# Kernel tuning notes

Hardware: AMD Instinct MI355X
Metric: run time of the kernel (lower is better)

Reference implementation:

```python
import jax, jax.numpy as jnp
import numpy as np

H, KVH, HD = 16, 8, 64
EPS = 1e-6
SCALING = HD ** -0.5


def _rms_norm(x, w):
    # RMSNorm over last dim (head_dim)
    var = jnp.mean(x * x, axis=-1, keepdims=True)
    return x * jax.lax.rsqrt(var + EPS) * w


def _rotate_half(x):
    x1, x2 = jnp.split(x, 2, axis=-1)
    return jnp.concatenate([-x2, x1], axis=-1)


def setup_inputs() -> dict:
    key = jax.random.key(0)
    ks = jax.random.split(key, 12)
    B, Q, CTX, HID = 1, 2048, 2048, 1024
    NB, T = 32, 64  # Q == NB * T
    TOTAL = CTX + Q
    inp = {}
    inp["hidden_states"] = jax.random.normal(ks[0], (B, Q, HID), jnp.float32)
    inp["target_hidden"] = jax.random.normal(ks[1], (B, CTX, HID), jnp.float32)
    pos = jnp.arange(TOTAL, dtype=jnp.float32)[:, None]
    inv = 1.0 / (10000.0 ** (jnp.arange(0, HD, 2, dtype=jnp.float32) / HD))
    ang = pos * inv[None, :]
    emb = jnp.concatenate([ang, ang], axis=-1)
    inp["cos"] = jnp.cos(emb)[None]  # [B, TOTAL, HD]
    inp["sin"] = jnp.sin(emb)[None]
    inp["attention_mask"] = jnp.zeros((B, 1, Q, TOTAL), jnp.float32)
    s = 0.02
    inp["Wq"] = jax.random.normal(ks[2], (HID, H * HD), jnp.float32) * s
    inp["Wk"] = jax.random.normal(ks[3], (HID, KVH * HD), jnp.float32) * s
    inp["Wv"] = jax.random.normal(ks[4], (HID, KVH * HD), jnp.float32) * s
    inp["Wo"] = jax.random.normal(ks[5], (H * HD, HID), jnp.float32) * s
    inp["q_norm_w"] = jnp.ones((HD,), jnp.float32)
    inp["k_norm_w"] = jnp.ones((HD,), jnp.float32)
    inp["tree_bias"] = jax.random.normal(ks[6], (64, H), jnp.float32) * s
    inp["relation_map"] = jax.random.randint(ks[7], (B, NB, T, T), 0, 64, jnp.int32)
    return inp


def reference(hidden_states, target_hidden, cos, sin, attention_mask,
              Wq, Wk, Wv, Wo, q_norm_w, k_norm_w, tree_bias, relation_map):
    B, Q, HID = hidden_states.shape
    CTX = target_hidden.shape[1]
    TOTAL = CTX + Q
    NB, T = relation_map.shape[1], relation_map.shape[2]
    groups = H // KVH

    q = (hidden_states @ Wq).reshape(B, Q, H, HD)
    k_ctx = target_hidden @ Wk
    k_noise = hidden_states @ Wk
    v_ctx = target_hidden @ Wv
    v_noise = hidden_states @ Wv
    k = jnp.concatenate([k_ctx, k_noise], axis=1).reshape(B, TOTAL, KVH, HD)
    v = jnp.concatenate([v_ctx, v_noise], axis=1).reshape(B, TOTAL, KVH, HD)

    q = _rms_norm(q, q_norm_w).transpose(0, 2, 1, 3)  # [B,H,Q,HD]
    k = _rms_norm(k, k_norm_w).transpose(0, 2, 1, 3)  # [B,KVH,TOTAL,HD]
    v = v.transpose(0, 2, 1, 3)

    cos_b = cos[:, None]  # [B,1,TOTAL,HD]
    sin_b = sin[:, None]
    q = q * cos_b[..., -Q:, :] + _rotate_half(q) * sin_b[..., -Q:, :]
    k = k * cos_b + _rotate_half(k) * sin_b

    # GQA: repeat kv heads
    k = jnp.repeat(k, groups, axis=1)  # [B,H,TOTAL,HD]
    v = jnp.repeat(v, groups, axis=1)

    scores = jnp.einsum('bhqd,bhkd->bhqk', q, k) * SCALING  # [B,H,Q,TOTAL]
    scores = scores + attention_mask

    # tree positional bias: block-diagonal (same tree) on the noise-noise block
    bias = tree_bias[relation_map]                 # [B,NB,T,T,H]
    bias = jnp.transpose(bias, (0, 4, 1, 2, 3))    # [B,H,NB,T,T]
    s_noise = scores[..., CTX:].reshape(B, H, NB, T, NB, T)
    idx = jnp.arange(NB)
    s_noise = s_noise.at[:, :, idx, :, idx, :].add(jnp.transpose(bias, (2, 0, 1, 3, 4)))
    scores = jnp.concatenate([scores[..., :CTX], s_noise.reshape(B, H, Q, Q)], axis=-1)

    attn = jax.nn.softmax(scores, axis=-1)
    out = jnp.einsum('bhqk,bhkd->bhqd', attn, v)   # [B,H,Q,HD]
    out = out.transpose(0, 2, 1, 3).reshape(B, Q, H * HD)
    return out @ Wo
```

## Files before the change

kernel.cpp:

```cpp
#include <hip/hip_runtime.h>
#include <hip/hip_bf16.h>

typedef __bf16 bf16x8 __attribute__((ext_vector_type(8)));
typedef float  f32x4  __attribute__((ext_vector_type(4)));

__device__ inline unsigned short f2bf(float f) {
    unsigned int u = __float_as_uint(f);
    u += 0x7fffu + ((u >> 16) & 1u);
    return (unsigned short)(u >> 16);
}
__device__ inline float bf2f(unsigned int s) {
    return __uint_as_float(s << 16);
}
__device__ inline unsigned int pk2bf(float a, float b) {
    __hip_bfloat162 h = __float22bfloat162_rn(make_float2(a, b));
    union { __hip_bfloat162 h; unsigned int u; } cv;
    cv.h = h;
    return cv.u;
}
__device__ inline f32x4 mfma16(bf16x8 a, bf16x8 b, f32x4 c) {
    return __builtin_amdgcn_mfma_f32_16x16x32_bf16(a, b, c, 0, 0, 0);
}
__device__ inline void gload_lds16(const void* g, void* l) {
    __builtin_amdgcn_global_load_lds(
        (const __attribute__((address_space(1))) void*)g,
        (__attribute__((address_space(3))) void*)l, 16, 0, 0);
}

__global__ __launch_bounds__(256) void cast2_bf(const float* __restrict__ a,
                                                const float* __restrict__ b,
                                                unsigned short* __restrict__ out, int n4each) {
    int i = blockIdx.x * 256 + threadIdx.x;
    float4 v = (i < n4each) ? ((const float4*)a)[i] : ((const float4*)b)[i - n4each];
    ((uint2*)out)[i] = make_uint2(pk2bf(v.x, v.y), pk2bf(v.z, v.w));
}

__global__ __launch_bounds__(256) void trans4v(const float* __restrict__ Wk,
                                               const float* __restrict__ Wv,
                                               const float* __restrict__ Wq,
                                               const float* __restrict__ Wo,
                                               unsigned short* __restrict__ Wkvt,
                                               unsigned short* __restrict__ Wqt,
                                               unsigned short* __restrict__ Wot) {
    __shared__ float t[64][65];
    int z = blockIdx.z;
    const float* in;
    unsigned short* out;
    int in_rs;
    if (z == 0)      { if (blockIdx.x >= 8) return; in = Wk; out = Wkvt; in_rs = 512; }
    else if (z == 1) { if (blockIdx.x >= 8) return; in = Wv; out = Wkvt + (size_t)512 * 1024; in_rs = 512; }
    else if (z == 2) { in = Wq; out = Wqt; in_rs = 1024; }
    else             { in = Wo; out = Wot; in_rs = 1024; }
    int r0 = blockIdx.y * 64, c0b = blockIdx.x * 64;
    int tid = threadIdx.x, rr = tid >> 4, c4 = (tid & 15) * 4;
#pragma unroll
    for (int i = 0; i < 4; i++) {
        int r = rr + 16 * i;
        float4 v = *(const float4*)&in[(size_t)(r0 + r) * in_rs + c0b + c4];
        t[c4][r] = v.x; t[c4 + 1][r] = v.y; t[c4 + 2][r] = v.z; t[c4 + 3][r] = v.w;
    }
    __syncthreads();
#pragma unroll
    for (int i = 0; i < 4; i++) {
        int cc = rr + 16 * i;
        *(uint2*)&out[(size_t)(c0b + cc) * 1024 + r0 + c4] =
            make_uint2(pk2bf(t[cc][c4], t[cc][c4 + 1]), pk2bf(t[cc][c4 + 2], t[cc][c4 + 3]));
    }
}

__global__ __launch_bounds__(256) void vtrans2(const unsigned short* __restrict__ in,
                                               unsigned short* __restrict__ out) {
    __shared__ float t[64][65];
    const unsigned short* ip = in + (size_t)blockIdx.y * 64 + (size_t)blockIdx.x * 64 * 1024;
    unsigned short* op = out + (size_t)blockIdx.y * 64 * 4096 + blockIdx.x * 64;
    int tid = threadIdx.x, rr = tid >> 4, c0 = (tid & 15) * 4;
#pragma unroll
    for (int i = 0; i < 4; i++) {
        int r = rr + 16 * i;
        uint2 v = *(const uint2*)&ip[(size_t)r * 1024 + c0];
        t[c0][r] = bf2f(v.x & 0xffff); t[c0 + 1][r] = bf2f(v.x >> 16);
        t[c0 + 2][r] = bf2f(v.y & 0xffff); t[c0 + 3][r] = bf2f(v.y >> 16);
    }
    __syncthreads();
#pragma unroll
    for (int i = 0; i < 4; i++) {
        int d = rr + 16 * i;
        *(uint2*)&op[(size_t)d * 4096 + c0] =
            make_uint2(pk2bf(t[d][c0], t[d][c0 + 1]), pk2bf(t[d][c0 + 2], t[d][c0 + 3]));
    }
}

template <bool BF16OUT>
__device__ inline void gemm64_body(const unsigned short* __restrict__ A,
                                   const unsigned short* __restrict__ Bt,
                                   void* __restrict__ C, int m0, int n0,
                                   unsigned short (*Al)[128 * 32],
                                   unsigned short (*Bl)[64 * 32]) {
    int tid = threadIdx.x, wave = tid >> 6, lane = tid & 63, quad = lane >> 4, l16 = lane & 15;
    f32x4 acc[2][4] = {};

    int dr = lane >> 2;
    int sch = ((lane & 3) ^ (dr & 3)) * 8;
    const unsigned short* Ag0 = A + (size_t)(m0 + 32 * wave + dr) * 1024 + sch;
    const unsigned short* Ag1 = A + (size_t)(m0 + 32 * wave + 16 + dr) * 1024 + sch;
    const unsigned short* Bg  = Bt + (size_t)(n0 + 16 * wave + dr) * 1024 + sch;

    auto dma = [&](int k0, int b) {
        gload_lds16(Ag0 + k0, (char*)Al[b] + wave * 2048);
        gload_lds16(Ag1 + k0, (char*)Al[b] + wave * 2048 + 1024);
        gload_lds16(Bg + k0, (char*)Bl[b] + wave * 1024);
    };
    dma(0, 0);
    int swz = (quad ^ (l16 & 3)) * 8;

    for (int k0 = 0; k0 < 1024; k0 += 32) {
        __syncthreads();
        int b = (k0 >> 5) & 1;
        if (k0 + 32 < 1024) dma(k0 + 32, b ^ 1);
        bf16x8 af[2], bq[4];
#pragma unroll
        for (int i = 0; i < 2; i++)
            af[i] = *(const bf16x8*)&Al[b][(wave * 32 + i * 16 + l16) * 32 + swz];
#pragma unroll
        for (int j = 0; j < 4; j++)
            bq[j] = *(const bf16x8*)&Bl[b][(j * 16 + l16) * 32 + swz];
#pragma unroll
        for (int i = 0; i < 2; i++)
#pragma unroll
            for (int j = 0; j < 4; j++)
                acc[i][j] = mfma16(af[i], bq[j], acc[i][j]);
    }
#pragma unroll
    for (int i = 0; i < 2; i++)
#pragma unroll
        for (int j = 0; j < 4; j++) {
            int m = m0 + wave * 32 + i * 16 + quad * 4;
            int n = n0 + j * 16 + l16;
#pragma unroll
            for (int r = 0; r < 4; r++) {
                if constexpr (BF16OUT)
                    ((unsigned short*)C)[(size_t)(m + r) * 1024 + n] = f2bf(acc[i][j][r]);
                else
                    ((float*)C)[(size_t)(m + r) * 1024 + n] = acc[i][j][r];
            }
        }
}

__global__ __launch_bounds__(256) void gemm_qkv(const unsigned short* __restrict__ X,
                                                const unsigned short* __restrict__ Wkvt,
                                                const unsigned short* __restrict__ Wqt,
                                                unsigned short* __restrict__ KVraw,
                                                unsigned short* __restrict__ Qraw) {
    __shared__ unsigned short Al[2][128 * 32];
    __shared__ unsigned short Bl[2][64 * 32];
    int bx = blockIdx.x, n0 = blockIdx.y * 64;
    if (bx < 32) gemm64_body<true>(X, Wkvt, KVraw, bx * 128, n0, Al, Bl);
    else         gemm64_body<true>(X + (size_t)2048 * 1024, Wqt, Qraw, (bx - 32) * 128, n0, Al, Bl);
}

__global__ __launch_bounds__(256) void gemm_wo(const unsigned short* __restrict__ A,
                                               const unsigned short* __restrict__ Bt,
                                               float* __restrict__ C) {
    __shared__ unsigned short Al[2][128 * 32];
    __shared__ unsigned short Bl[2][64 * 32];
    gemm64_body<false>(A, Bt, C, blockIdx.x * 128, blockIdx.y * 64, Al, Bl);
}

__global__ __launch_bounds__(256) void norm_rope3(const unsigned short* __restrict__ Qraw,
                                                  const unsigned short* __restrict__ KVraw,
                                                  const float* __restrict__ qw,
                                                  const float* __restrict__ kw,
                                                  const float* __restrict__ cosb,
                                                  const float* __restrict__ sinb,
                                                  unsigned short* __restrict__ Qb,
                                                  unsigned short* __restrict__ Kb) {
    int gw = (blockIdx.x * 256 + threadIdx.x) >> 6;
    int lane = threadIdx.x & 63;
    int hl = lane >> 4, d0 = (lane & 15) * 4;
    const unsigned short* src;
    unsigned short* dst;
    const float* w;
    int pos;
    float scale;
    if (gw < 8192) {
        int r = gw >> 2, seg = gw & 3, h = seg * 4 + hl;
        src = Qraw + (size_t)r * 1024 + h * 64 + d0;
        dst = Qb + ((size_t)h * 2048 + r) * 64 + d0;
        w = qw; pos = 2048 + r; scale = 0.18033688011112042f;
    } else {
        int g2 = gw - 8192;
        int r = g2 >> 1, seg = g2 & 1, h = seg * 4 + hl;
        src = KVraw + (size_t)r * 1024 + h * 64 + d0;
        dst = Kb + ((size_t)h * 4096 + r) * 64 + d0;
        w = kw; pos = r; scale = 1.0f;
    }
    uint2 raw = *(const uint2*)src;
    float x0 = bf2f(raw.x & 0xffff), x1 = bf2f(raw.x >> 16);
    float x2 = bf2f(raw.y & 0xffff), x3 = bf2f(raw.y >> 16);
    float ss = x0 * x0 + x1 * x1 + x2 * x2 + x3 * x3;
    ss += __shfl_xor(ss, 1); ss += __shfl_xor(ss, 2);
    ss += __shfl_xor(ss, 4); ss += __shfl_xor(ss, 8);
    float rn = rsqrtf(ss * (1.0f / 64.0f) + 1e-6f);
    float4 wv = *(const float4*)(w + d0);
    float xn0 = x0 * rn * wv.x, xn1 = x1 * rn * wv.y;
    float xn2 = x2 * rn * wv.z, xn3 = x3 * rn * wv.w;
    float o0 = __shfl_xor(xn0, 8), o1 = __shfl_xor(xn1, 8);
    float o2 = __shfl_xor(xn2, 8), o3 = __shfl_xor(xn3, 8);
    float sgn = (d0 < 32) ? -1.0f : 1.0f;
    float4 cv = *(const float4*)(cosb + (size_t)pos * 64 + d0);
    float4 sv = *(const float4*)(sinb + (size_t)pos * 64 + d0);
    float y0 = fmaf(xn0, cv.x, sgn * o0 * sv.x) * scale;
    float y1 = fmaf(xn1, cv.y, sgn * o1 * sv.y) * scale;
    float y2 = fmaf(xn2, cv.z, sgn * o2 * sv.z) * scale;
    float y3 = fmaf(xn3, cv.w, sgn * o3 * sv.w) * scale;
    *(uint2*)dst = make_uint2(pk2bf(y0, y1), pk2bf(y2, y3));
}

__global__ __launch_bounds__(256) void attn4(const unsigned short* __restrict__ Qb,
                                             const unsigned short* __restrict__ Kb,
                                             const unsigned short* __restrict__ Vt,
                                             const int* __restrict__ relmap,
                                             const float* __restrict__ tree_bias,
                                             unsigned short* __restrict__ Opart,
                                             float* __restrict__ Lpart) {
    __shared__ alignas(16) union {
        struct { unsigned short K[2][4096]; unsigned short V[2][4096]; unsigned short P[4][32 * 72]; } s;
        unsigned short O[128 * 72];
    } u;

    int qt = blockIdx.x, h = blockIdx.y, ks = blockIdx.z, kvh = h >> 1;
    int tid = threadIdx.x, wave = tid >> 6, lane = tid & 63, quad = lane >> 4, l16 = lane & 15;

    bf16x8 qf[2][2];
#pragma unroll
    for (int qg = 0; qg < 2; qg++) {
        int q = qt * 128 + wave * 32 + qg * 16 + l16;
        const unsigned short* qp = Qb + ((size_t)h * 2048 + q) * 64 + quad * 8;
        qf[qg][0] = *(const bf16x8*)qp;
        qf[qg][1] = *(const bf16x8*)(qp + 32);
    }
    f32x4 o[4][2] = {};
    f32x4 lacc[2] = {};

    union { unsigned short us[8]; bf16x8 v; } one_u;
#pragma unroll
    for (int i = 0; i < 8; i++) one_u.us[i] = 0x3F80;
    const bf16x8 ones = one_u.v;

    int drow = lane >> 3;
    int sch = ((lane & 7) ^ drow) * 8;
    const unsigned short* KgB = Kb + ((size_t)kvh * 4096 + ks * 1024) * 64;
    const unsigned short* VgB = Vt + (size_t)kvh * 64 * 4096 + ks * 1024;
    int r0 = wave * 16, r1 = wave * 16 + 8;
    const unsigned short* Kg0 = KgB + (size_t)(r0 + drow) * 64 + sch;
    const unsigned short* Kg1 = KgB + (size_t)(r1 + drow) * 64 + sch;
    const unsigned short* Vg0 = VgB + (size_t)(r0 + drow) * 4096 + sch;
    const unsigned short* Vg1 = VgB + (size_t)(r1 + drow) * 4096 + sch;

    auto dma = [&](int kt, int b) {
        gload_lds16(Kg0 + kt * 4096, &u.s.K[b][r0 * 64]);
        gload_lds16(Kg1 + kt * 4096, &u.s.K[b][r1 * 64]);
        gload_lds16(Vg0 + kt * 64, &u.s.V[b][r0 * 64]);
        gload_lds16(Vg1 + kt * 64, &u.s.V[b][r1 * 64]);
    };
    dma(0, 0);

    unsigned short* pw = &u.s.P[wave][0];
    int sw = l16 & 7;
    int nb = 2 * qt + (wave >> 1);
    int bias_kt = 32 + nb - ks * 16;
    const float LOG2E = 1.4426950408889634f;

    for (int kt = 0; kt < 16; kt++) {
        __syncthreads();
        int b = kt & 1;
        if (kt + 1 < 16) dma(kt + 1, b ^ 1);

#pragma unroll
        for (int half = 0; half < 2; half++) {
            float pvv[2][2][4];
#pragma unroll
            for (int gl = 0; gl < 2; gl++) {
                int g = half * 2 + gl;
                int krow = (g * 16 + l16) * 64;
                bf16x8 kf0 = *(const bf16x8*)&u.s.K[b][krow + ((quad ^ sw) * 8)];
                bf16x8 kf1 = *(const bf16x8*)&u.s.K[b][krow + (((4 + quad) ^ sw) * 8)];
#pragma unroll
                for (int qg = 0; qg < 2; qg++) {
                    f32x4 s = {};
                    s = mfma16(kf0, qf[qg][0], s);
                    s = mfma16(kf1, qf[qg][1], s);
#pragma unroll
                    for (int r = 0; r < 4; r++) pvv[gl][qg][r] = s[r];
                }
            }
            if (kt == bias_kt) {
#pragma unroll
                for (int gl = 0; gl < 2; gl++)
#pragma unroll
                    for (int qg = 0; qg < 2; qg++)
#pragma unroll
                        for (int r = 0; r < 4; r++) {
                            int t1 = (wave & 1) * 32 + qg * 16 + l16;
                            int t2 = (half * 2 + gl) * 16 + quad * 4 + r;
                            int rel = relmap[nb * 4096 + t1 * 64 + t2];
                            pvv[gl][qg][r] += tree_bias[rel * 16 + h] * LOG2E;
                        }
            }
#pragma unroll
            for (int gl = 0; gl < 2; gl++)
#pragma unroll
                for (int qg = 0; qg < 2; qg++) {
                    float p0 = __builtin_amdgcn_exp2f(pvv[gl][qg][0]);
                    float p1 = __builtin_amdgcn_exp2f(pvv[gl][qg][1]);
                    float p2 = __builtin_amdgcn_exp2f(pvv[gl][qg][2]);
                    float p3 = __builtin_amdgcn_exp2f(pvv[gl][qg][3]);
                    *(uint2*)&pw[(qg * 16 + l16) * 72 + (half * 2 + gl) * 16 + quad * 4] =
                        make_uint2(pk2bf(p0, p1), pk2bf(p2, p3));
                }
#pragma unroll
            for (int qg = 0; qg < 2; qg++) {
                bf16x8 pf = *(const bf16x8*)&pw[(qg * 16 + l16) * 72 + half * 32 + quad * 8];
                lacc[qg] = mfma16(ones, pf, lacc[qg]);
#pragma unroll
                for (int dg = 0; dg < 4; dg++) {
                    int vrow = (dg * 16 + l16) * 64;
                    bf16x8 vf = *(const bf16x8*)&u.s.V[b][vrow + (((half * 4 + quad) ^ sw) * 8)];
                    o[dg][qg] = mfma16(vf, pf, o[dg][qg]);
                }
            }
        }
    }
    __syncthreads();

    float lv0 = lacc[0][0], lv1 = lacc[1][0];
#pragma unroll
    for (int qg = 0; qg < 2; qg++) {
        int qlocal = wave * 32 + qg * 16 + l16;
#pragma unroll
        for (int dg = 0; dg < 4; dg++) {
            f32x4 ov = o[dg][qg];
            *(uint2*)&u.O[qlocal * 72 + dg * 16 + quad * 4] =
                make_uint2(pk2bf(ov[0], ov[1]), pk2bf(ov[2], ov[3]));
        }
        if (quad == 0)
            Lpart[((size_t)ks * 16 + h) * 2048 + qt * 128 + qlocal] = qg ? lv1 : lv0;
    }
    __syncthreads();
    int row = tid >> 3, c = (tid & 7) * 8;
#pragma unroll
    for (int i = 0; i < 4; i++) {
        int rr = row + 32 * i;
        uint4 val = *(uint4*)&u.O[rr * 72 + c];
        size_t q = qt * 128 + rr;
        *(uint4*)&Opart[((size_t)ks * 2048 + q) * 1024 + h * 64 + c] = val;
    }
}

__global__ __launch_bounds__(256) void combine4(const unsigned short* __restrict__ Op,
                                                const float* __restrict__ Lp,
                                                unsigned short* __restrict__ AO) {
    int t = blockIdx.x * 256 + threadIdx.x;
    int q = t >> 7, h = (t >> 3) & 15, c8 = (t & 7) * 8;
    size_t base = ((size_t)q * 16 + h) * 64 + c8;
    float s[8] = {};
    float l = 0.0f;
#pragma unroll
    for (int ks = 0; ks < 4; ks++) {
        uint4 v = *(const uint4*)&Op[(size_t)ks * 2097152 + base];
        s[0] += bf2f(v.x & 0xffff); s[1] += bf2f(v.x >> 16);
        s[2] += bf2f(v.y & 0xffff); s[3] += bf2f(v.y >> 16);
        s[4] += bf2f(v.z & 0xffff); s[5] += bf2f(v.z >> 16);
        s[6] += bf2f(v.w & 0xffff); s[7] += bf2f(v.w >> 16);
        l += Lp[((size_t)ks * 16 + h) * 2048 + q];
    }
    float inv = 1.0f / l;
    uint4 r;
    r.x = pk2bf(s[0] * inv, s[1] * inv);
    r.y = pk2bf(s[2] * inv, s[3] * inv);
    r.z = pk2bf(s[4] * inv, s[5] * inv);
    r.w = pk2bf(s[6] * inv, s[7] * inv);
    *(uint4*)&AO[base] = r;
}

extern "C" void kernel_launch(void* const* d_in, const int* in_sizes, int n_in,
                              void* d_out, int out_size, void* d_ws, size_t ws_size,
                              hipStream_t stream) {
    const float* hs   = (const float*)d_in[0];
    const float* th   = (const float*)d_in[1];
    const float* cosb = (const float*)d_in[2];
    const float* sinb = (const float*)d_in[3];
    const float* Wq  = (const float*)d_in[5];
    const float* Wk  = (const float*)d_in[6];
    const float* Wv  = (const float*)d_in[7];
    const float* Wo  = (const float*)d_in[8];
    const float* qnw = (const float*)d_in[9];
    const float* knw = (const float*)d_in[10];
    const float* tb  = (const float*)d_in[11];
    const int*   rm  = (const int*)d_in[12];
    float* out = (float*)d_out;

    char* ws = (char*)d_ws;
    size_t off = 0;
    auto alloc = [&](size_t b) { char* p = ws + off; off += (b + 255) & ~(size_t)255; return p; };
    unsigned short* X     = (unsigned short*)alloc((size_t)4096 * 1024 * 2);
    unsigned short* Qrawb = (unsigned short*)alloc((size_t)2048 * 1024 * 2);
    unsigned short* KVraw = (unsigned short*)alloc((size_t)4096 * 1024 * 2);
    unsigned short* Wqt   = (unsigned short*)alloc((size_t)1024 * 1024 * 2);
    unsigned short* Wkvt  = (unsigned short*)alloc((size_t)1024 * 1024 * 2);
    unsigned short* Wot   = (unsigned short*)alloc((size_t)1024 * 1024 * 2);
    unsigned short* Qb    = (unsigned short*)alloc((size_t)16 * 2048 * 64 * 2);
    unsigned short* Kb    = (unsigned short*)alloc((size_t)8 * 4096 * 64 * 2);
    unsigned short* Vtr   = (unsigned short*)alloc((size_t)8 * 64 * 4096 * 2);
    unsigned short* AOb   = (unsigned short*)alloc((size_t)2048 * 1024 * 2);
    float*          Lpart = (float*)alloc((size_t)4 * 16 * 2048 * 4);
    unsigned short* Opart = X;

    cast2_bf<<<4096, 256, 0, stream>>>(th, hs, X, 2048 * 1024 / 4);
    trans4v<<<dim3(16, 16, 4), 256, 0, stream>>>(Wk, Wv, Wq, Wo, Wkvt, Wqt, Wot);
    gemm_qkv<<<dim3(48, 16), 256, 0, stream>>>(X, Wkvt, Wqt, KVraw, Qrawb);
    norm_rope3<<<4096, 256, 0, stream>>>(Qrawb, KVraw, qnw, knw, cosb, sinb, Qb, Kb);
    vtrans2<<<dim3(64, 8), 256, 0, stream>>>(KVraw + 512, Vtr);
    attn4<<<dim3(16, 16, 4), 256, 0, stream>>>(Qb, Kb, Vtr, rm, tb, Opart, Lpart);
    combine4<<<1024, 256, 0, stream>>>(Opart, Lpart, AOb);
    gemm_wo<<<dim3(16, 16), 256, 0, stream>>>(AOb, Wot, out);
}
```

Before: 228.3 us.

## Merge prep kernels and load V fragments directly from global in attention

Result: slower. 262.7 us (+15.1%).

```diff
diff --git a/kernel.cpp b/kernel.cpp
--- a/kernel.cpp
+++ b/kernel.cpp
@@ -27,32 +27,30 @@
         (__attribute__((address_space(3))) void*)l, 16, 0, 0);
 }
 
-__global__ __launch_bounds__(256) void cast2_bf(const float* __restrict__ a,
-                                                const float* __restrict__ b,
-                                                unsigned short* __restrict__ out, int n4each) {
-    int i = blockIdx.x * 256 + threadIdx.x;
-    float4 v = (i < n4each) ? ((const float4*)a)[i] : ((const float4*)b)[i - n4each];
-    ((uint2*)out)[i] = make_uint2(pk2bf(v.x, v.y), pk2bf(v.z, v.w));
-}
-
-__global__ __launch_bounds__(256) void trans4v(const float* __restrict__ Wk,
-                                               const float* __restrict__ Wv,
-                                               const float* __restrict__ Wq,
-                                               const float* __restrict__ Wo,
-                                               unsigned short* __restrict__ Wkvt,
-                                               unsigned short* __restrict__ Wqt,
-                                               unsigned short* __restrict__ Wot) {
+__global__ __launch_bounds__(256) void prep1(const float* __restrict__ th, const float* __restrict__ hs,
+                                             const float* __restrict__ Wk, const float* __restrict__ Wv,
+                                             const float* __restrict__ Wq, const float* __restrict__ Wo,
+                                             unsigned short* __restrict__ X,
+                                             unsigned short* __restrict__ Wkvt,
+                                             unsigned short* __restrict__ Wqt,
+                                             unsigned short* __restrict__ Wot) {
     __shared__ float t[64][65];
-    int z = blockIdx.z;
-    const float* in;
-    unsigned short* out;
-    int in_rs;
-    if (z == 0)      { if (blockIdx.x >= 8) return; in = Wk; out = Wkvt; in_rs = 512; }
-    else if (z == 1) { if (blockIdx.x >= 8) return; in = Wv; out = Wkvt + (size_t)512 * 1024; in_rs = 512; }
-    else if (z == 2) { in = Wq; out = Wqt; in_rs = 1024; }
-    else             { in = Wo; out = Wot; in_rs = 1024; }
-    int r0 = blockIdx.y * 64, c0b = blockIdx.x * 64;
-    int tid = threadIdx.x, rr = tid >> 4, c4 = (tid & 15) * 4;
+    int bx = blockIdx.x, tid = threadIdx.x;
+    if (bx < 4096) {
+        int i = bx * 256 + tid;
+        const int n4 = 2048 * 1024 / 4;
+        float4 v = (i < n4) ? ((const float4*)th)[i] : ((const float4*)hs)[i - n4];
+        ((uint2*)X)[i] = make_uint2(pk2bf(v.x, v.y), pk2bf(v.z, v.w));
+        return;
+    }
+    int t4 = bx - 4096;
+    const float* in; unsigned short* out; int in_rs, xt, yt;
+    if (t4 < 256)      { in = Wq; out = Wqt; in_rs = 1024; xt = t4 & 15; yt = t4 >> 4; }
+    else if (t4 < 512) { t4 -= 256; in = Wo; out = Wot; in_rs = 1024; xt = t4 & 15; yt = t4 >> 4; }
+    else if (t4 < 640) { t4 -= 512; in = Wk; out = Wkvt; in_rs = 512; xt = t4 & 7; yt = t4 >> 3; }
+    else               { t4 -= 640; in = Wv; out = Wkvt + (size_t)512 * 1024; in_rs = 512; xt = t4 & 7; yt = t4 >> 3; }
+    int r0 = yt * 64, c0b = xt * 64;
+    int rr = tid >> 4, c4 = (tid & 15) * 4;
 #pragma unroll
     for (int i = 0; i < 4; i++) {
         int r = rr + 16 * i;
@@ -68,34 +66,12 @@
     }
 }
 
-__global__ __launch_bounds__(256) void vtrans2(const unsigned short* __restrict__ in,
-                                               unsigned short* __restrict__ out) {
-    __shared__ float t[64][65];
-    const unsigned short* ip = in + (size_t)blockIdx.y * 64 + (size_t)blockIdx.x * 64 * 1024;
-    unsigned short* op = out + (size_t)blockIdx.y * 64 * 4096 + blockIdx.x * 64;
-    int tid = threadIdx.x, rr = tid >> 4, c0 = (tid & 15) * 4;
-#pragma unroll
-    for (int i = 0; i < 4; i++) {
-        int r = rr + 16 * i;
-        uint2 v = *(const uint2*)&ip[(size_t)r * 1024 + c0];
-        t[c0][r] = bf2f(v.x & 0xffff); t[c0 + 1][r] = bf2f(v.x >> 16);
-        t[c0 + 2][r] = bf2f(v.y & 0xffff); t[c0 + 3][r] = bf2f(v.y >> 16);
-    }
-    __syncthreads();
-#pragma unroll
-    for (int i = 0; i < 4; i++) {
-        int d = rr + 16 * i;
-        *(uint2*)&op[(size_t)d * 4096 + c0] =
-            make_uint2(pk2bf(t[d][c0], t[d][c0 + 1]), pk2bf(t[d][c0 + 2], t[d][c0 + 3]));
-    }
-}
-
 template <bool BF16OUT>
-__device__ inline void gemm64_body(const unsigned short* __restrict__ A,
-                                   const unsigned short* __restrict__ Bt,
-                                   void* __restrict__ C, int m0, int n0,
-                                   unsigned short (*Al)[128 * 32],
-                                   unsigned short (*Bl)[64 * 32]) {
+__device__ __forceinline__ void gemm64_body(const unsigned short* __restrict__ A,
+                                            const unsigned short* __restrict__ Bt,
+                                            void* __restrict__ C, int m0, int n0,
+                                            unsigned short (*Al)[128 * 32],
+                                            unsigned short (*Bl)[64 * 32]) {
     int tid = threadIdx.x, wave = tid >> 6, lane = tid & 63, quad = lane >> 4, l16 = lane & 15;
     f32x4 acc[2][4] = {};
 
@@ -166,65 +142,90 @@
     gemm64_body<false>(A, Bt, C, blockIdx.x * 128, blockIdx.y * 64, Al, Bl);
 }
 
-__global__ __launch_bounds__(256) void norm_rope3(const unsigned short* __restrict__ Qraw,
-                                                  const unsigned short* __restrict__ KVraw,
-                                                  const float* __restrict__ qw,
-                                                  const float* __restrict__ kw,
-                                                  const float* __restrict__ cosb,
-                                                  const float* __restrict__ sinb,
-                                                  unsigned short* __restrict__ Qb,
-                                                  unsigned short* __restrict__ Kb) {
-    int gw = (blockIdx.x * 256 + threadIdx.x) >> 6;
-    int lane = threadIdx.x & 63;
-    int hl = lane >> 4, d0 = (lane & 15) * 4;
-    const unsigned short* src;
-    unsigned short* dst;
-    const float* w;
-    int pos;
-    float scale;
-    if (gw < 8192) {
-        int r = gw >> 2, seg = gw & 3, h = seg * 4 + hl;
-        src = Qraw + (size_t)r * 1024 + h * 64 + d0;
-        dst = Qb + ((size_t)h * 2048 + r) * 64 + d0;
-        w = qw; pos = 2048 + r; scale = 0.18033688011112042f;
-    } else {
-        int g2 = gw - 8192;
-        int r = g2 >> 1, seg = g2 & 1, h = seg * 4 + hl;
-        src = KVraw + (size_t)r * 1024 + h * 64 + d0;
-        dst = Kb + ((size_t)h * 4096 + r) * 64 + d0;
-        w = kw; pos = r; scale = 1.0f;
-    }
-    uint2 raw = *(const uint2*)src;
-    float x0 = bf2f(raw.x & 0xffff), x1 = bf2f(raw.x >> 16);
-    float x2 = bf2f(raw.y & 0xffff), x3 = bf2f(raw.y >> 16);
-    float ss = x0 * x0 + x1 * x1 + x2 * x2 + x3 * x3;
-    ss += __shfl_xor(ss, 1); ss += __shfl_xor(ss, 2);
-    ss += __shfl_xor(ss, 4); ss += __shfl_xor(ss, 8);
-    float rn = rsqrtf(ss * (1.0f / 64.0f) + 1e-6f);
-    float4 wv = *(const float4*)(w + d0);
-    float xn0 = x0 * rn * wv.x, xn1 = x1 * rn * wv.y;
-    float xn2 = x2 * rn * wv.z, xn3 = x3 * rn * wv.w;
-    float o0 = __shfl_xor(xn0, 8), o1 = __shfl_xor(xn1, 8);
-    float o2 = __shfl_xor(xn2, 8), o3 = __shfl_xor(xn3, 8);
-    float sgn = (d0 < 32) ? -1.0f : 1.0f;
-    float4 cv = *(const float4*)(cosb + (size_t)pos * 64 + d0);
-    float4 sv = *(const float4*)(sinb + (size_t)pos * 64 + d0);
-    float y0 = fmaf(xn0, cv.x, sgn * o0 * sv.x) * scale;
-    float y1 = fmaf(xn1, cv.y, sgn * o1 * sv.y) * scale;
-    float y2 = fmaf(xn2, cv.z, sgn * o2 * sv.z) * scale;
-    float y3 = fmaf(xn3, cv.w, sgn * o3 * sv.w) * scale;
-    *(uint2*)dst = make_uint2(pk2bf(y0, y1), pk2bf(y2, y3));
-}
-
-__global__ __launch_bounds__(256) void attn4(const unsigned short* __restrict__ Qb,
-                                             const unsigned short* __restrict__ Kb,
-                                             const unsigned short* __restrict__ Vt,
-                                             const int* __restrict__ relmap,
-                                             const float* __restrict__ tree_bias,
-                                             unsigned short* __restrict__ Opart,
-                                             float* __restrict__ Lpart) {
+__global__ __launch_bounds__(256) void prep2(const unsigned short* __restrict__ Qraw,
+                                             const unsigned short* __restrict__ KVraw,
+                                             const float* __restrict__ qw, const float* __restrict__ kw,
+                                             const float* __restrict__ cosb, const float* __restrict__ sinb,
+                                             unsigned short* __restrict__ Qb,
+                                             unsigned short* __restrict__ Kb,
+                                             unsigned short* __restrict__ Vtr) {
+    __shared__ float t[64][65];
+    int bx = blockIdx.x, tid = threadIdx.x;
+    if (bx < 4096) {
+        int gw = (bx * 256 + tid) >> 6;
+        int lane = tid & 63;
+        int hl = lane >> 4, d0 = (lane & 15) * 4;
+        const unsigned short* src;
+        unsigned short* dst;
+        const float* w;
+        int pos;
+        float scale;
+        if (gw < 8192) {
+            int r = gw >> 2, seg = gw & 3, h = seg * 4 + hl;
+            src = Qraw + (size_t)r * 1024 + h * 64 + d0;
+            dst = Qb + ((size_t)h * 2048 + r) * 64 + d0;
+            w = qw; pos = 2048 + r; scale = 0.18033688011112042f;
+        } else {
+            int g2 = gw - 8192;
+            int r = g2 >> 1, seg = g2 & 1, h = seg * 4 + hl;
+            src = KVraw + (size_t)r * 1024 + h * 64 + d0;
+            dst = Kb + ((size_t)h * 4096 + r) * 64 + d0;
+            w = kw; pos = r; scale = 1.0f;
+        }
+        uint2 raw = *(const uint2*)src;
+        float x0 = bf2f(raw.x & 0xffff), x1 = bf2f(raw.x >> 16);
+        float x2 = bf2f(raw.y & 0xffff), x3 = bf2f(raw.y >> 16);
+        float ss = x0 * x0 + x1 * x1 + x2 * x2 + x3 * x3;
+        ss += __shfl_xor(ss, 1); ss += __shfl_xor(ss, 2);
+        ss += __shfl_xor(ss, 4); ss += __shfl_xor(ss, 8);
+        float rn = rsqrtf(ss * (1.0f / 64.0f) + 1e-6f);
+        float4 wv = *(const float4*)(w + d0);
+        float xn0 = x0 * rn * wv.x, xn1 = x1 * rn * wv.y;
+        float xn2 = x2 * rn * wv.z, xn3 = x3 * rn * wv.w;
+        float o0 = __shfl_xor(xn0, 8), o1 = __shfl_xor(xn1, 8);
+        float o2 = __shfl_xor(xn2, 8), o3 = __shfl_xor(xn3, 8);
+        float sgn = (d0 < 32) ? -1.0f : 1.0f;
+        float4 cv = *(const float4*)(cosb + (size_t)pos * 64 + d0);
+        float4 sv = *(const float4*)(sinb + (size_t)pos * 64 + d0);
+        float y0 = fmaf(xn0, cv.x, sgn * o0 * sv.x) * scale;
+        float y1 = fmaf(xn1, cv.y, sgn * o1 * sv.y) * scale;
+        float y2 = fmaf(xn2, cv.z, sgn * o2 * sv.z) * scale;
+        float y3 = fmaf(xn3, cv.w, sgn * o3 * sv.w) * scale;
+        *(uint2*)dst = make_uint2(pk2bf(y0, y1), pk2bf(y2, y3));
+        return;
+    }
+    int t4 = bx - 4096;
+    int xk = t4 & 63, z = t4 >> 6;
+    const unsigned short* ip = KVraw + (size_t)xk * 64 * 1024 + 512 + z * 64;
+    unsigned short* op = Vtr + (size_t)z * 64 * 4096 + (size_t)xk * 64;
+    int rr = tid >> 4, c0 = (tid & 15) * 4;
+#pragma unroll
+    for (int i = 0; i < 4; i++) {
+        int r = rr + 16 * i;
+        uint2 v = *(const uint2*)&ip[(size_t)r * 1024 + c0];
+        t[c0][r]     = bf2f(v.x & 0xffff);
+        t[c0 + 1][r] = bf2f(v.x >> 16);
+        t[c0 + 2][r] = bf2f(v.y & 0xffff);
+        t[c0 + 3][r] = bf2f(v.y >> 16);
+    }
+    __syncthreads();
+#pragma unroll
+    for (int i = 0; i < 4; i++) {
+        int d = rr + 16 * i;
+        *(uint2*)&op[(size_t)d * 4096 + c0] =
+            make_uint2(pk2bf(t[d][c0], t[d][c0 + 1]), pk2bf(t[d][c0 + 2], t[d][c0 + 3]));
+    }
+}
+
+__global__ __launch_bounds__(256, 4) void attn6(const unsigned short* __restrict__ Qb,
+                                                const unsigned short* __restrict__ Kb,
+                                                const unsigned short* __restrict__ Vt,
+                                                const int* __restrict__ relmap,
+                                                const float* __restrict__ tree_bias,
+                                                unsigned short* __restrict__ Opart,
+                                                float* __restrict__ Lpart) {
     __shared__ alignas(16) union {
-        struct { unsigned short K[2][4096]; unsigned short V[2][4096]; unsigned short P[4][32 * 72]; } s;
+        struct { unsigned short K[2][4096]; unsigned short P[4][2048]; } s;
         unsigned short O[128 * 72];
     } u;
 
@@ -241,7 +242,6 @@
     }
     f32x4 o[4][2] = {};
     f32x4 lacc[2] = {};
-
     union { unsigned short us[8]; bf16x8 v; } one_u;
 #pragma unroll
     for (int i = 0; i < 8; i++) one_u.us[i] = 0x3F80;
@@ -250,86 +250,87 @@
     int drow = lane >> 3;
     int sch = ((lane & 7) ^ drow) * 8;
     const unsigned short* KgB = Kb + ((size_t)kvh * 4096 + ks * 1024) * 64;
-    const unsigned short* VgB = Vt + (size_t)kvh * 64 * 4096 + ks * 1024;
-    int r0 = wave * 16, r1 = wave * 16 + 8;
+    int r0 = wave * 16, r1 = r0 + 8;
     const unsigned short* Kg0 = KgB + (size_t)(r0 + drow) * 64 + sch;
     const unsigned short* Kg1 = KgB + (size_t)(r1 + drow) * 64 + sch;
-    const unsigned short* Vg0 = VgB + (size_t)(r0 + drow) * 4096 + sch;
-    const unsigned short* Vg1 = VgB + (size_t)(r1 + drow) * 4096 + sch;
-
-    auto dma = [&](int kt, int b) {
-        gload_lds16(Kg0 + kt * 4096, &u.s.K[b][r0 * 64]);
-        gload_lds16(Kg1 + kt * 4096, &u.s.K[b][r1 * 64]);
-        gload_lds16(Vg0 + kt * 64, &u.s.V[b][r0 * 64]);
-        gload_lds16(Vg1 + kt * 64, &u.s.V[b][r1 * 64]);
-    };
-    dma(0, 0);
+
+    const unsigned short* Vg = Vt + ((size_t)kvh * 64 + l16) * 4096 + ks * 1024 + quad * 8;
+
+    gload_lds16(Kg0, &u.s.K[0][r0 * 64]);
+    gload_lds16(Kg1, &u.s.K[0][r1 * 64]);
 
     unsigned short* pw = &u.s.P[wave][0];
     int sw = l16 & 7;
+    int psw = (l16 & 7) * 2;
     int nb = 2 * qt + (wave >> 1);
     int bias_kt = 32 + nb - ks * 16;
     const float LOG2E = 1.4426950408889634f;
 
     for (int kt = 0; kt < 16; kt++) {
+        int b = kt & 1;
         __syncthreads();
-        int b = kt & 1;
-        if (kt + 1 < 16) dma(kt + 1, b ^ 1);
-
-#pragma unroll
-        for (int half = 0; half < 2; half++) {
-            float pvv[2][2][4];
-#pragma unroll
-            for (int gl = 0; gl < 2; gl++) {
-                int g = half * 2 + gl;
-                int krow = (g * 16 + l16) * 64;
-                bf16x8 kf0 = *(const bf16x8*)&u.s.K[b][krow + ((quad ^ sw) * 8)];
-                bf16x8 kf1 = *(const bf16x8*)&u.s.K[b][krow + (((4 + quad) ^ sw) * 8)];
-#pragma unroll
-                for (int qg = 0; qg < 2; qg++) {
-                    f32x4 s = {};
-                    s = mfma16(kf0, qf[qg][0], s);
-                    s = mfma16(kf1, qf[qg][1], s);
-#pragma unroll
-                    for (int r = 0; r < 4; r++) pvv[gl][qg][r] = s[r];
-                }
+        if (kt + 1 < 16) {
+            gload_lds16(Kg0 + (kt + 1) * 4096, &u.s.K[b ^ 1][r0 * 64]);
+            gload_lds16(Kg1 + (kt + 1) * 4096, &u.s.K[b ^ 1][r1 * 64]);
+        }
+        bf16x8 vf[4][2];
+#pragma unroll
+        for (int dg = 0; dg < 4; dg++) {
+            const unsigned short* vp = Vg + (size_t)(dg * 16) * 4096 + kt * 64;
+            vf[dg][0] = *(const bf16x8*)vp;
+            vf[dg][1] = *(const bf16x8*)(vp + 32);
+        }
+
+#pragma unroll
+        for (int g = 0; g < 4; g++) {
+            int krow = (g * 16 + l16) * 64;
+            bf16x8 kf0 = *(const bf16x8*)&u.s.K[b][krow + ((quad ^ sw) * 8)];
+            bf16x8 kf1 = *(const bf16x8*)&u.s.K[b][krow + (((4 + quad) ^ sw) * 8)];
+            float pv[2][4];
+#pragma unroll
+            for (int qg = 0; qg < 2; qg++) {
+                f32x4 s = {};
+                s = mfma16(kf0, qf[qg][0], s);
+                s = mfma16(kf1, qf[qg][1], s);
+#pragma unroll
+                for (int r = 0; r < 4; r++) pv[qg][r] = s[r];
             }
             if (kt == bias_kt) {
 #pragma unroll
-                for (int gl = 0; gl < 2; gl++)
-#pragma unroll
-                    for (int qg = 0; qg < 2; qg++)
-#pragma unroll
-                        for (int r = 0; r < 4; r++) {
-                            int t1 = (wave & 1) * 32 + qg * 16 + l16;
-                            int t2 = (half * 2 + gl) * 16 + quad * 4 + r;
-                            int rel = relmap[nb * 4096 + t1 * 64 + t2];
-                            pvv[gl][qg][r] += tree_bias[rel * 16 + h] * LOG2E;
-                        }
+                for (int qg = 0; qg < 2; qg++)
+#pragma unroll
+                    for (int r = 0; r < 4; r++) {
+                        int t1 = (wave & 1) * 32 + qg * 16 + l16;
+                        int t2 = g * 16 + quad * 4 + r;
+                        int rel = relmap[nb * 4096 + t1 * 64 + t2];
+                        pv[qg][r] += tree_bias[rel * 16 + h] * LOG2E;
+                    }
             }
 #pragma unroll
-            for (int gl = 0; gl < 2; gl++)
-#pragma unroll
-                for (int qg = 0; qg < 2; qg++) {
-                    float p0 = __builtin_amdgcn_exp2f(pvv[gl][qg][0]);
-                    float p1 = __builtin_amdgcn_exp2f(pvv[gl][qg][1]);
-                    float p2 = __builtin_amdgcn_exp2f(pvv[gl][qg][2]);
-                    float p3 = __builtin_amdgcn_exp2f(pvv[gl][qg][3]);
-                    *(uint2*)&pw[(qg * 16 + l16) * 72 + (half * 2 + gl) * 16 + quad * 4] =
-                        make_uint2(pk2bf(p0, p1), pk2bf(p2, p3));
-                }
-#pragma unroll
             for (int qg = 0; qg < 2; qg++) {
-                bf16x8 pf = *(const bf16x8*)&pw[(qg * 16 + l16) * 72 + half * 32 + quad * 8];
-                lacc[qg] = mfma16(ones, pf, lacc[qg]);
-#pragma unroll
-                for (int dg = 0; dg < 4; dg++) {
-                    int vrow = (dg * 16 + l16) * 64;
-                    bf16x8 vf = *(const bf16x8*)&u.s.V[b][vrow + (((half * 4 + quad) ^ sw) * 8)];
-                    o[dg][qg] = mfma16(vf, pf, o[dg][qg]);
-                }
+                float p0 = __builtin_amdgcn_exp2f(pv[qg][0]);
+                float p1 = __builtin_amdgcn_exp2f(pv[qg][1]);
+                float p2 = __builtin_amdgcn_exp2f(pv[qg][2]);
+                float p3 = __builtin_amdgcn_exp2f(pv[qg][3]);
+                *(uint2*)&pw[(qg * 16 + l16) * 64 + (((g * 4 + quad) ^ psw) * 4)] =
+                    make_uint2(pk2bf(p0, p1), pk2bf(p2, p3));
             }
         }
+        bf16x8 pf[2][2];
+#pragma unroll
+        for (int qg = 0; qg < 2; qg++) {
+            pf[qg][0] = *(const bf16x8*)&pw[(qg * 16 + l16) * 64 + (((quad * 2) ^ psw) * 4)];
+            pf[qg][1] = *(const bf16x8*)&pw[(qg * 16 + l16) * 64 + (((8 + quad * 2) ^ psw) * 4)];
+            lacc[qg] = mfma16(ones, pf[qg][0], lacc[qg]);
+            lacc[qg] = mfma16(ones, pf[qg][1], lacc[qg]);
+        }
+#pragma unroll
+        for (int dg = 0; dg < 4; dg++)
+#pragma unroll
+            for (int qg = 0; qg < 2; qg++) {
+                o[dg][qg] = mfma16(vf[dg][0], pf[qg][0], o[dg][qg]);
+                o[dg][qg] = mfma16(vf[dg][1], pf[qg][1], o[dg][qg]);
+            }
     }
     __syncthreads();
 
@@ -416,12 +417,10 @@
     float*          Lpart = (float*)alloc((size_t)4 * 16 * 2048 * 4);
     unsigned short* Opart = X;
 
-    cast2_bf<<<4096, 256, 0, stream>>>(th, hs, X, 2048 * 1024 / 4);
-    trans4v<<<dim3(16, 16, 4), 256, 0, stream>>>(Wk, Wv, Wq, Wo, Wkvt, Wqt, Wot);
+    prep1<<<4864, 256, 0, stream>>>(th, hs, Wk, Wv, Wq, Wo, X, Wkvt, Wqt, Wot);
     gemm_qkv<<<dim3(48, 16), 256, 0, stream>>>(X, Wkvt, Wqt, KVraw, Qrawb);
-    norm_rope3<<<4096, 256, 0, stream>>>(Qrawb, KVraw, qnw, knw, cosb, sinb, Qb, Kb);
-    vtrans2<<<dim3(64, 8), 256, 0, stream>>>(KVraw + 512, Vtr);
-    attn4<<<dim3(16, 16, 4), 256, 0, stream>>>(Qb, Kb, Vtr, rm, tb, Opart, Lpart);
+    prep2<<<4608, 256, 0, stream>>>(Qrawb, KVraw, qnw, knw, cosb, sinb, Qb, Kb, Vtr);
+    attn6<<<dim3(16, 16, 4), 256, 0, stream>>>(Qb, Kb, Vtr, rm, tb, Opart, Lpart);
     combine4<<<1024, 256, 0, stream>>>(Opart, Lpart, AOb);
     gemm_wo<<<dim3(16, 16), 256, 0, stream>>>(AOb, Wot, out);
 }
```
